# Kernel tuning notes

Measured on AMD Instinct MI355X. Metric: run time of the kernel, lower is better.

Reference implementation:

```python
import jax, jax.numpy as jnp
import numpy as np

N, D, H, DK, DEG = 8192, 512, 8, 64, 16
E = N * DEG
M = N


def setup_inputs() -> dict:
    key = jax.random.key(0)
    ks = jax.random.split(key, 12)
    x = jax.random.normal(ks[0], (N, D), dtype=jnp.float32)
    # every node has DEG neighbors -> sorted row index, random cols
    row_index = jnp.repeat(jnp.arange(N, dtype=jnp.int64), DEG)
    col_index = jax.random.randint(ks[1], (E,), 0, M, dtype=jnp.int64)
    to_col_index = jax.random.randint(ks[2], (M,), 0, N, dtype=jnp.int64)
    att_bias = 0.1 * jax.random.normal(ks[3], (H, E), dtype=jnp.float32)
    pos = 10.0 * jax.random.uniform(ks[4], (N, 3), dtype=jnp.float32)
    col_pos = 10.0 * jax.random.uniform(ks[5], (M, 3), dtype=jnp.float32)
    dist = jnp.linalg.norm(col_pos[col_index] - pos[row_index], axis=-1)
    s = 1.0 / np.sqrt(D)
    Wq = s * jax.random.normal(ks[6], (H, DK, D), dtype=jnp.float32)
    Wqv = s * jax.random.normal(ks[7], (H, 3, D), dtype=jnp.float32)
    Wk = s * jax.random.normal(ks[8], (H, DK, D), dtype=jnp.float32)
    Wv = s * jax.random.normal(ks[9], (H, DK, D), dtype=jnp.float32)
    Wout = s * jax.random.normal(ks[10], (D, D + 4 * H), dtype=jnp.float32)
    bout = jnp.zeros((D,), dtype=jnp.float32)
    return {"x": x, "row_index": row_index, "col_index": col_index,
            "to_col_index": to_col_index, "att_bias": att_bias, "dist": dist,
            "pos": pos, "col_pos": col_pos, "Wq": Wq, "Wqv": Wqv, "Wk": Wk,
            "Wv": Wv, "Wout": Wout, "bout": bout}


def reference(x, row_index, col_index, to_col_index, att_bias, dist, pos,
              col_pos, Wq, Wqv, Wk, Wv, Wout, bout):
    n = x.shape[0]
    dk = Wq.shape[1]
    scale = 1.0 / jnp.sqrt(jnp.asarray(dk, x.dtype))
    # per-head projections: [H, N, dk]
    q = jnp.einsum('nd,hkd->hnk', x, Wq) * scale
    qv = jnp.einsum('nd,hkd->hnk', x, Wqv)              # [H, N, 3]
    kx = jnp.einsum('nd,hkd->hnk', x, Wk)[:, to_col_index]  # [H, M, dk]
    vx = jnp.einsum('nd,hkd->hnk', x, Wv)[:, to_col_index]
    # gather per edge -> [E, H, *]
    qe = q[:, row_index].transpose(1, 0, 2)
    ke = kx[:, col_index].transpose(1, 0, 2)
    qve = qv[:, row_index].transpose(1, 0, 2)           # [E, H, 3]
    rel = col_pos[col_index] - pos[row_index]           # [E, 3]
    dist_e = jnp.where(dist == 0, jnp.inf, dist)        # masked_fill(dist==0, inf)
    # angular = qv_row . col_pos_col - qv_row . pos_row = qv_row . rel
    angular = jnp.einsum('ehc,ec->eh', qve, rel)
    logit = jnp.einsum('ehk,ehk->eh', qe, ke) + att_bias.T + angular / dist_e[:, None]
    # sparse (per-row segment) softmax
    m = jax.ops.segment_max(logit, row_index, num_segments=n)
    p = jnp.exp(logit - m[row_index])
    s = jax.ops.segment_sum(p, row_index, num_segments=n)
    att = p / s[row_index]                              # [E, H]
    natt = att / dist_e[:, None]
    dst_vec = jax.ops.segment_sum(natt[:, :, None] * col_pos[col_index][:, None, :],
                                  row_index, num_segments=n)   # [N, H, 3]
    avg_inv_dist = jax.ops.segment_sum(natt, row_index, num_segments=n)  # [N, H]
    src_vec = avg_inv_dist[:, :, None] * pos[:, None, :]
    diff = dst_vec - src_vec
    feat3 = diff / jnp.maximum(jnp.linalg.norm(diff, axis=-1, keepdims=True), 1e-12)
    ve = vx[:, col_index].transpose(1, 0, 2)            # [E, H, dk]
    y = jax.ops.segment_sum(att[:, :, None] * ve, row_index, num_segments=n)  # [N, H, dk]
    feat = jnp.concatenate([y, feat3, avg_inv_dist[:, :, None]], axis=-1)
    feat = feat.reshape(n, -1)                          # [N, H*(dk+4)]
    return feat @ Wout.T + bout
```

## Files before the change

kernel.cpp:

```cpp
#include <hip/hip_runtime.h>
#include <math.h>

#define N_NODES 8192
#define D_FEAT  512
#define DEG     16
#define E_EDGES (N_NODES * DEG)
#define FEAT_W  576
#define FEAT_USED 544
#define OUT_W   512
#define QKV_W   1664

typedef unsigned short u16;
typedef __attribute__((ext_vector_type(8))) short short8;
typedef __attribute__((ext_vector_type(8))) unsigned short us8;
typedef __attribute__((ext_vector_type(4))) float f32x4;

__device__ __forceinline__ u16 f2bf(float f) {
    union { float f; unsigned u; } c; c.f = f;
    unsigned u = c.u;
    unsigned r = u + 0x7FFFu + ((u >> 16) & 1u);
    return (u16)(r >> 16);
}
__device__ __forceinline__ float bf2f(u16 h) {
    union { unsigned u; float f; } c; c.u = ((unsigned)h) << 16;
    return c.f;
}

__device__ __forceinline__ void async16(const void* g, void* l) {
    __builtin_amdgcn_global_load_lds(
        (const __attribute__((address_space(1))) void*)g,
        (__attribute__((address_space(3))) void*)l, 16, 0, 0);
}

__global__ __launch_bounds__(256) void gemm_qkv(
    const u16* __restrict__ xh, const u16* __restrict__ Bfuse,
    u16* __restrict__ qkv)
{
    __shared__ u16 smem[128 * 64 * 2];
    u16* sA = smem;
    u16* sB = smem + 128 * 64;

    const int tid = threadIdx.x;
    const int flat = blockIdx.x;
    const int xcd = flat & 7;
    const int rr  = flat >> 3;
    const int bm  = (xcd + 8 * (rr / 13)) * 128;
    const int bn  = (rr % 13) * 128;

    const int wave = tid >> 6;
    const int lane = tid & 63;
    const int wr   = (wave >> 1) * 64;
    const int wc   = (wave & 1) * 64;
    const int lrow = lane & 15;
    const int quad = lane >> 4;

    f32x4 acc[4][4];
    #pragma unroll
    for (int i = 0; i < 4; ++i)
        #pragma unroll
        for (int j = 0; j < 4; ++j) {
            f32x4 z = {0.f, 0.f, 0.f, 0.f};
            acc[i][j] = z;
        }

    for (int k0 = 0; k0 < 512; k0 += 64) {
        #pragma unroll
        for (int i = 0; i < 4; ++i) {
            const int lin = i * 256 + tid;
            const int row = lin >> 3;
            const int seg = ((lin & 7) ^ (row & 7)) << 3;
            async16(xh    + (size_t)(bm + row) * 512 + k0 + seg, sA + (lin << 3));
            async16(Bfuse + (size_t)(bn + row) * 512 + k0 + seg, sB + (lin << 3));
        }
        __syncthreads();

        #pragma unroll
        for (int ko = 0; ko < 64; ko += 32) {
            const int cbase = ko >> 3;
            short8 a_h[4], b_h[4];
            #pragma unroll
            for (int t = 0; t < 4; ++t) {
                const int ra = wr + t * 16 + lrow;
                const int rb = wc + t * 16 + lrow;
                a_h[t] = *(const short8*)&sA[ra * 64 + (((cbase + quad) ^ (ra & 7)) << 3)];
                b_h[t] = *(const short8*)&sB[rb * 64 + (((cbase + quad) ^ (rb & 7)) << 3)];
            }
            #pragma unroll
            for (int mt = 0; mt < 4; ++mt)
                #pragma unroll
                for (int nt = 0; nt < 4; ++nt)
                    acc[mt][nt] = __builtin_amdgcn_mfma_f32_16x16x32_bf16(
                        a_h[mt], b_h[nt], acc[mt][nt], 0, 0, 0);
        }
        __syncthreads();
    }

    #pragma unroll
    for (int nt = 0; nt < 4; ++nt) {
        const int col = bn + wc + nt * 16 + lrow;
        #pragma unroll
        for (int mt = 0; mt < 4; ++mt)
            #pragma unroll
            for (int r = 0; r < 4; ++r) {
                const int row = bm + wr + mt * 16 + quad * 4 + r;
                qkv[(size_t)row * QKV_W + col] = f2bf(acc[mt][nt][r]);
            }
    }
}

__global__ __launch_bounds__(256) void gemm_out(
    const u16* __restrict__ feat, const u16* __restrict__ Woth,
    const float* __restrict__ bout, float* __restrict__ out)
{
    __shared__ u16 smem[64 * 64 + 128 * 64];
    u16* sA = smem;
    u16* sB = smem + 64 * 64;

    const int tid = threadIdx.x;
    const int flat = blockIdx.x;
    const int xcd = flat & 7;
    const int rr  = flat >> 3;
    const int bm  = (xcd + 8 * (rr / 4)) * 64;
    const int bn  = (rr % 4) * 128;

    const int wave = tid >> 6;
    const int lane = tid & 63;
    const int wr   = (wave >> 1) * 32;
    const int wc   = (wave & 1) * 64;
    const int lrow = lane & 15;
    const int quad = lane >> 4;

    f32x4 acc[2][4];
    #pragma unroll
    for (int i = 0; i < 2; ++i)
        #pragma unroll
        for (int j = 0; j < 4; ++j) {
            f32x4 z = {0.f, 0.f, 0.f, 0.f};
            acc[i][j] = z;
        }

    for (int k0 = 0; k0 < FEAT_W; k0 += 64) {
        #pragma unroll
        for (int i = 0; i < 2; ++i) {
            const int lin = i * 256 + tid;
            const int row = lin >> 3;
            const int seg = ((lin & 7) ^ (row & 7)) << 3;
            async16(feat + (size_t)(bm + row) * FEAT_W + k0 + seg, sA + (lin << 3));
        }
        #pragma unroll
        for (int i = 0; i < 4; ++i) {
            const int lin = i * 256 + tid;
            const int row = lin >> 3;
            const int seg = ((lin & 7) ^ (row & 7)) << 3;
            async16(Woth + (size_t)(bn + row) * FEAT_W + k0 + seg, sB + (lin << 3));
        }
        __syncthreads();

        #pragma unroll
        for (int ko = 0; ko < 64; ko += 32) {
            const int cbase = ko >> 3;
            short8 a_h[2], b_h[4];
            #pragma unroll
            for (int t = 0; t < 2; ++t) {
                const int ra = wr + t * 16 + lrow;
                a_h[t] = *(const short8*)&sA[ra * 64 + (((cbase + quad) ^ (ra & 7)) << 3)];
            }
            #pragma unroll
            for (int t = 0; t < 4; ++t) {
                const int rb = wc + t * 16 + lrow;
                b_h[t] = *(const short8*)&sB[rb * 64 + (((cbase + quad) ^ (rb & 7)) << 3)];
            }
            #pragma unroll
            for (int mt = 0; mt < 2; ++mt)
                #pragma unroll
                for (int nt = 0; nt < 4; ++nt)
                    acc[mt][nt] = __builtin_amdgcn_mfma_f32_16x16x32_bf16(
                        a_h[mt], b_h[nt], acc[mt][nt], 0, 0, 0);
        }
        __syncthreads();
    }

    #pragma unroll
    for (int nt = 0; nt < 4; ++nt) {
        const int col = bn + wc + nt * 16 + lrow;
        const float bb = bout[col];
        #pragma unroll
        for (int mt = 0; mt < 2; ++mt)
            #pragma unroll
            for (int r = 0; r < 4; ++r) {
                const int row = bm + wr + mt * 16 + quad * 4 + r;
                out[(size_t)row * OUT_W + col] = acc[mt][nt][r] + bb;
            }
    }
}

__global__ __launch_bounds__(256) void prep_kernel(
    const float* __restrict__ x,
    const float* __restrict__ Wq, const float* __restrict__ Wk,
    const float* __restrict__ Wv, const float* __restrict__ Wqv,
    const float* __restrict__ Wout,
    u16* __restrict__ xh, u16* __restrict__ B, u16* __restrict__ Woth)
{
    const int b = blockIdx.x;
    const int tid = threadIdx.x;
    if (b < 4096) {
        const int i = b * 256 + tid;
        const float4 v = ((const float4*)x)[i];
        ushort4 h;
        h.x = f2bf(v.x); h.y = f2bf(v.y); h.z = f2bf(v.z); h.w = f2bf(v.w);
        ((ushort4*)xh)[i] = h;
    } else if (b < 4928) {
        const int idx = (b - 4096) * 256 + tid;
        const int row = idx >> 7;
        const int c4  = idx & 127;
        float4 v = make_float4(0.f, 0.f, 0.f, 0.f);
        float scale = 1.f;
        if (row < 512) {
            v = *(const float4*)(Wq + (size_t)row * 512 + c4 * 4);
            scale = 0.125f;
        } else if (row < 1024) {
            v = *(const float4*)(Wk + (size_t)(row - 512) * 512 + c4 * 4);
        } else if (row < 1536) {
            v = *(const float4*)(Wv + (size_t)(row - 1024) * 512 + c4 * 4);
        } else if (row < 1560) {
            v = *(const float4*)(Wqv + (size_t)(row - 1536) * 512 + c4 * 4);
        }
        ushort4 h;
        h.x = f2bf(v.x * scale); h.y = f2bf(v.y * scale);
        h.z = f2bf(v.z * scale); h.w = f2bf(v.w * scale);
        ((ushort4*)B)[idx] = h;
    } else {
        const int i = (b - 4928) * 256 + tid;
        const int row = i / (FEAT_W / 4);
        const int c4  = i % (FEAT_W / 4);
        float4 v = make_float4(0.f, 0.f, 0.f, 0.f);
        if (c4 < FEAT_USED / 4)
            v = *(const float4*)(Wout + (size_t)row * FEAT_USED + c4 * 4);
        ushort4 h;
        h.x = f2bf(v.x); h.y = f2bf(v.y); h.z = f2bf(v.z); h.w = f2bf(v.w);
        ((ushort4*)Woth)[i] = h;
    }
}

__global__ __launch_bounds__(256) void edge_kernel(
    const u16* __restrict__ qkv,
    const int* __restrict__ col_index, const int* __restrict__ to_col,
    const float* __restrict__ att_bias, const float* __restrict__ dist,
    const float* __restrict__ pos, const float* __restrict__ col_pos,
    u16* __restrict__ feat)
{
    __shared__ float sLog[2][2][8][8];
    __shared__ float sY[2][512];
    __shared__ float sV[2][8][4];

    const int wave4 = threadIdx.x >> 6;
    const int nb = wave4 >> 1;
    const int w  = wave4 & 1;
    const int lane = threadIdx.x & 63;
    const int n = blockIdx.x * 2 + nb;
    const int h = lane >> 3;
    const int sub = lane & 7;
    const int hoff = lane * 8;

    const size_t qbase = (size_t)n * QKV_W;

    float qf[8];
    {
        const us8 qu = *(const us8*)(qkv + qbase + hoff);
        #pragma unroll
        for (int i = 0; i < 8; ++i) qf[i] = bf2f(qu[i]);
    }
    float qv0, qv1, qv2;
    {
        const float qvl = bf2f(qkv[qbase + 1536 + (lane < 24 ? lane : 0)]);
        qv0 = __shfl(qvl, h * 3 + 0);
        qv1 = __shfl(qvl, h * 3 + 1);
        qv2 = __shfl(qvl, h * 3 + 2);
    }
    const float px = pos[3 * n + 0], py = pos[3 * n + 1], pz = pos[3 * n + 2];

    const int j8 = lane & 7;
    const int e0 = n * DEG + w * 8 + j8;
    const int c_l  = col_index[e0];
    const int cc_l = to_col[c_l];
    const float d_l = dist[e0];
    const float invd_l = (d_l == 0.f) ? 0.f : (1.f / d_l);
    const float rx_l = col_pos[3 * c_l + 0] - px;
    const float ry_l = col_pos[3 * c_l + 1] - py;
    const float rz_l = col_pos[3 * c_l + 2] - pz;

    const float b_own = att_bias[(size_t)h * E_EDGES + n * DEG + w * 8 + sub];

    float logit[8];
    #pragma unroll
    for (int j = 0; j < 8; ++j) {
        const int cc = __shfl(cc_l, j);
        const us8 ku = *(const us8*)(qkv + (size_t)cc * QKV_W + 512 + hoff);
        float dot = 0.f;
        #pragma unroll
        for (int i = 0; i < 8; ++i) dot += qf[i] * bf2f(ku[i]);
        dot += __shfl_xor(dot, 1, 8);
        dot += __shfl_xor(dot, 2, 8);
        dot += __shfl_xor(dot, 4, 8);
        const float invd = __shfl(invd_l, j);
        const float ang = qv0 * __shfl(rx_l, j) + qv1 * __shfl(ry_l, j)
                        + qv2 * __shfl(rz_l, j);
        const float bj = __shfl(b_own, j, 8);
        logit[j] = dot + bj + ang * invd;
    }

    if (sub == 0) {
        #pragma unroll
        for (int j = 0; j < 8; ++j) sLog[nb][w][h][j] = logit[j];
    }
    __syncthreads();
    float lo[8];
    #pragma unroll
    for (int j = 0; j < 8; ++j) lo[j] = sLog[nb][1 - w][h][j];

    float m = logit[0];
    #pragma unroll
    for (int j = 1; j < 8; ++j) m = fmaxf(m, logit[j]);
    #pragma unroll
    for (int j = 0; j < 8; ++j) m = fmaxf(m, lo[j]);
    float s = 0.f;
    #pragma unroll
    for (int j = 0; j < 8; ++j) { logit[j] = __expf(logit[j] - m); s += logit[j]; }
    #pragma unroll
    for (int j = 0; j < 8; ++j) s += __expf(lo[j] - m);
    const float inv_s = 1.f / s;

    float y[8] = {0.f, 0.f, 0.f, 0.f, 0.f, 0.f, 0.f, 0.f};
    float dx = 0.f, dy = 0.f, dz = 0.f, aid = 0.f;
    #pragma unroll
    for (int j = 0; j < 8; ++j) {
        const float a = logit[j] * inv_s;
        const int cc = __shfl(cc_l, j);
        const us8 vu = *(const us8*)(qkv + (size_t)cc * QKV_W + 1024 + hoff);
        #pragma unroll
        for (int i = 0; i < 8; ++i) y[i] += a * bf2f(vu[i]);
        const float na = a * __shfl(invd_l, j);
        dx += na * __shfl(rx_l, j);
        dy += na * __shfl(ry_l, j);
        dz += na * __shfl(rz_l, j);
        aid += na;
    }

    if (w == 0) {
        #pragma unroll
        for (int i = 0; i < 8; ++i) sY[nb][hoff + i] = y[i];
        if (sub == 0) {
            sV[nb][h][0] = dx; sV[nb][h][1] = dy;
            sV[nb][h][2] = dz; sV[nb][h][3] = aid;
        }
    }
    __syncthreads();
    if (w == 1) {
        #pragma unroll
        for (int i = 0; i < 8; ++i) y[i] += sY[nb][hoff + i];

        u16* f = feat + (size_t)n * FEAT_W + h * 68;
        ushort4 o0, o1;
        o0.x = f2bf(y[0]); o0.y = f2bf(y[1]); o0.z = f2bf(y[2]); o0.w = f2bf(y[3]);
        o1.x = f2bf(y[4]); o1.y = f2bf(y[5]); o1.z = f2bf(y[6]); o1.w = f2bf(y[7]);
        *(ushort4*)(f + sub * 8 + 0) = o0;
        *(ushort4*)(f + sub * 8 + 4) = o1;
        if (sub == 0) {
            dx += sV[nb][h][0]; dy += sV[nb][h][1];
            dz += sV[nb][h][2]; aid += sV[nb][h][3];
            const float nrm = sqrtf(dx * dx + dy * dy + dz * dz);
            const float rn = 1.f / fmaxf(nrm, 1e-12f);
            ushort4 ex;
            ex.x = f2bf(dx * rn); ex.y = f2bf(dy * rn);
            ex.z = f2bf(dz * rn); ex.w = f2bf(aid);
            *(ushort4*)(f + 64) = ex;
        }
    }
}

extern "C" void kernel_launch(void* const* d_in, const int* in_sizes, int n_in,
                              void* d_out, int out_size, void* d_ws, size_t ws_size,
                              hipStream_t stream)
{
    const float* x         = (const float*)d_in[0];
    const int*   col_index = (const int*)d_in[2];
    const int*   to_col    = (const int*)d_in[3];
    const float* att_bias  = (const float*)d_in[4];
    const float* dist      = (const float*)d_in[5];
    const float* pos       = (const float*)d_in[6];
    const float* col_pos   = (const float*)d_in[7];
    const float* Wq        = (const float*)d_in[8];
    const float* Wqv       = (const float*)d_in[9];
    const float* Wk        = (const float*)d_in[10];
    const float* Wv        = (const float*)d_in[11];
    const float* Wout      = (const float*)d_in[12];
    const float* bout      = (const float*)d_in[13];
    float* out = (float*)d_out;

    char* ws = (char*)d_ws;
    u16* qkv   = (u16*)(ws + 0);
    u16* xh    = (u16*)(ws + 27262976);
    u16* Bfuse = (u16*)(ws + 35651584);
    u16* Woth  = (u16*)(ws + 37355520);
    u16* feat  = (u16*)(ws + 37945344);

    dim3 blk(256);

    hipLaunchKernelGGL(prep_kernel, dim3(5216), blk, 0, stream,
                       x, Wq, Wk, Wv, Wqv, Wout, xh, Bfuse, Woth);

    hipLaunchKernelGGL(gemm_qkv, dim3(832), blk, 0, stream, xh, Bfuse, qkv);

    hipLaunchKernelGGL(edge_kernel, dim3(N_NODES / 2), blk, 0, stream,
                       qkv, col_index, to_col, att_bias, dist, pos, col_pos, feat);

    hipLaunchKernelGGL(gemm_out, dim3(512), blk, 0, stream,
                       feat, Woth, bout, out);
}
```

Measured before the change: 163.9 us.

## Rewrite QKV GEMM with 256x256 tiles and 4-stage async LDS pipeline

The QKV projection GEMM moves from 128x128 tiles with 256 threads to 256x256 tiles with 512 threads. It adds a four-buffer global-to-LDS prefetch ring with explicit waitcnt and barrier scheduling, and raises wave priority around the MFMA bursts. The aim is to overlap global loads with matrix math, cut per-tile sync stalls, and increase operand reuse. The fused weight buffer is padded to 1792 rows so N divides by 256, which adds some wasted compute on the padding columns and increases register pressure.

```diff
diff --git a/kernel.cpp b/kernel.cpp
--- a/kernel.cpp
+++ b/kernel.cpp
@@ -9,6 +9,7 @@
 #define FEAT_USED 544
 #define OUT_W   512
 #define QKV_W   1664
+#define BF_ROWS 1792
 
 typedef unsigned short u16;
 typedef __attribute__((ext_vector_type(8))) short short8;
@@ -32,79 +33,128 @@
         (__attribute__((address_space(3))) void*)l, 16, 0, 0);
 }
 
-__global__ __launch_bounds__(256) void gemm_qkv(
+__global__ __launch_bounds__(512, 2) void gemm_qkv(
     const u16* __restrict__ xh, const u16* __restrict__ Bfuse,
     u16* __restrict__ qkv)
 {
-    __shared__ u16 smem[128 * 64 * 2];
-    u16* sA = smem;
-    u16* sB = smem + 128 * 64;
-
-    const int tid = threadIdx.x;
-    const int flat = blockIdx.x;
-    const int xcd = flat & 7;
-    const int rr  = flat >> 3;
-    const int bm  = (xcd + 8 * (rr / 13)) * 128;
-    const int bn  = (rr % 13) * 128;
-
-    const int wave = tid >> 6;
+    __shared__ u16 ldsA[4][256 * 32];
+    __shared__ u16 ldsB[4][256 * 32];
+
+    const int tid  = threadIdx.x;
+    const int wid  = tid >> 6;
     const int lane = tid & 63;
-    const int wr   = (wave >> 1) * 64;
-    const int wc   = (wave & 1) * 64;
+    const int wm   = wid >> 2;
+    const int wn   = wid & 3;
     const int lrow = lane & 15;
     const int quad = lane >> 4;
 
-    f32x4 acc[4][4];
-    #pragma unroll
-    for (int i = 0; i < 4; ++i)
+    const int flat = blockIdx.x;
+    const int wg   = (flat & 7) * 28 + (flat >> 3);
+    const int bm   = (wg / 7) * 256;
+    const int bn   = (wg % 7) * 256;
+
+    const u16* gA = xh    + (size_t)bm * 512;
+    const u16* gB = Bfuse + (size_t)bn * 512;
+
+    const int c0 = tid,       r0 = c0 >> 2;
+    const int c1 = 512 + tid, r1 = c1 >> 2;
+    const int o0 = (((c0 & 3) ^ ((r0 >> 1) & 3)) << 3);
+    const int o1 = (((c1 & 3) ^ ((r1 >> 1) & 3)) << 3);
+
+#define STAGE_A(s) do {                                                      \
+        u16* _d = &ldsA[(s) & 3][0];                                         \
+        async16(gA + (size_t)r0 * 512 + (s) * 32 + o0, _d + c0 * 8);         \
+        async16(gA + (size_t)r1 * 512 + (s) * 32 + o1, _d + c1 * 8);         \
+    } while (0)
+#define STAGE_B(s) do {                                                      \
+        u16* _d = &ldsB[(s) & 3][0];                                         \
+        async16(gB + (size_t)r0 * 512 + (s) * 32 + o0, _d + c0 * 8);         \
+        async16(gB + (size_t)r1 * 512 + (s) * 32 + o1, _d + c1 * 8);         \
+    } while (0)
+
+    f32x4 acc[8][4];
+    #pragma unroll
+    for (int i = 0; i < 8; ++i)
         #pragma unroll
         for (int j = 0; j < 4; ++j) {
             f32x4 z = {0.f, 0.f, 0.f, 0.f};
             acc[i][j] = z;
         }
 
-    for (int k0 = 0; k0 < 512; k0 += 64) {
-        #pragma unroll
-        for (int i = 0; i < 4; ++i) {
-            const int lin = i * 256 + tid;
-            const int row = lin >> 3;
-            const int seg = ((lin & 7) ^ (row & 7)) << 3;
-            async16(xh    + (size_t)(bm + row) * 512 + k0 + seg, sA + (lin << 3));
-            async16(Bfuse + (size_t)(bn + row) * 512 + k0 + seg, sB + (lin << 3));
-        }
-        __syncthreads();
-
-        #pragma unroll
-        for (int ko = 0; ko < 64; ko += 32) {
-            const int cbase = ko >> 3;
-            short8 a_h[4], b_h[4];
-            #pragma unroll
-            for (int t = 0; t < 4; ++t) {
-                const int ra = wr + t * 16 + lrow;
-                const int rb = wc + t * 16 + lrow;
-                a_h[t] = *(const short8*)&sA[ra * 64 + (((cbase + quad) ^ (ra & 7)) << 3)];
-                b_h[t] = *(const short8*)&sB[rb * 64 + (((cbase + quad) ^ (rb & 7)) << 3)];
-            }
-            #pragma unroll
-            for (int mt = 0; mt < 4; ++mt)
+    STAGE_A(0); STAGE_B(0);
+    STAGE_A(1); STAGE_B(1);
+    STAGE_A(2); STAGE_B(2);
+    asm volatile("s_waitcnt vmcnt(8)" ::: "memory");
+    __builtin_amdgcn_s_barrier();
+
+    #pragma unroll
+    for (int s = 0; s < 16; ++s) {
+        const int b = s & 3;
+        const u16* sa = &ldsA[b][0];
+        const u16* sb = &ldsB[b][0];
+        short8 av[4], bv[4], av2[4];
+
+        #pragma unroll
+        for (int m = 0; m < 4; ++m) {
+            const int row = wm * 128 + m * 16 + lrow;
+            av[m] = *(const short8*)&sa[row * 32 + ((quad ^ ((row >> 1) & 3)) << 3)];
+        }
+        #pragma unroll
+        for (int n = 0; n < 4; ++n) {
+            const int row = wn * 64 + n * 16 + lrow;
+            bv[n] = *(const short8*)&sb[row * 32 + ((quad ^ ((row >> 1) & 3)) << 3)];
+        }
+        if (s < 13) STAGE_A(s + 3);
+        __builtin_amdgcn_s_barrier();
+        asm volatile("s_waitcnt lgkmcnt(0)" ::: "memory");
+        __builtin_amdgcn_sched_barrier(0);
+        __builtin_amdgcn_s_setprio(1);
+        #pragma unroll
+        for (int m = 0; m < 4; ++m)
+            #pragma unroll
+            for (int n = 0; n < 4; ++n)
+                acc[m][n] = __builtin_amdgcn_mfma_f32_16x16x32_bf16(
+                    av[m], bv[n], acc[m][n], 0, 0, 0);
+        __builtin_amdgcn_s_setprio(0);
+        __builtin_amdgcn_s_barrier();
+
+        #pragma unroll
+        for (int m = 0; m < 4; ++m) {
+            const int row = wm * 128 + 64 + m * 16 + lrow;
+            av2[m] = *(const short8*)&sa[row * 32 + ((quad ^ ((row >> 1) & 3)) << 3)];
+        }
+        if (s < 13) STAGE_B(s + 3);
+        __builtin_amdgcn_s_barrier();
+        asm volatile("s_waitcnt lgkmcnt(0)" ::: "memory");
+        __builtin_amdgcn_sched_barrier(0);
+        __builtin_amdgcn_s_setprio(1);
+        #pragma unroll
+        for (int m = 0; m < 4; ++m)
+            #pragma unroll
+            for (int n = 0; n < 4; ++n)
+                acc[4 + m][n] = __builtin_amdgcn_mfma_f32_16x16x32_bf16(
+                    av2[m], bv[n], acc[4 + m][n], 0, 0, 0);
+        __builtin_amdgcn_s_setprio(0);
+        if (s < 13)       asm volatile("s_waitcnt vmcnt(8)" ::: "memory");
+        else if (s == 13) asm volatile("s_waitcnt vmcnt(4)" ::: "memory");
+        else if (s == 14) asm volatile("s_waitcnt vmcnt(0)" ::: "memory");
+        __builtin_amdgcn_s_barrier();
+    }
+#undef STAGE_A
+#undef STAGE_B
+
+    #pragma unroll
+    for (int np = 0; np < 4; ++np) {
+        const int col = bn + wn * 64 + np * 16 + lrow;
+        if (col < 1560) {
+            #pragma unroll
+            for (int mp = 0; mp < 8; ++mp)
                 #pragma unroll
-                for (int nt = 0; nt < 4; ++nt)
-                    acc[mt][nt] = __builtin_amdgcn_mfma_f32_16x16x32_bf16(
-                        a_h[mt], b_h[nt], acc[mt][nt], 0, 0, 0);
-        }
-        __syncthreads();
-    }
-
-    #pragma unroll
-    for (int nt = 0; nt < 4; ++nt) {
-        const int col = bn + wc + nt * 16 + lrow;
-        #pragma unroll
-        for (int mt = 0; mt < 4; ++mt)
-            #pragma unroll
-            for (int r = 0; r < 4; ++r) {
-                const int row = bm + wr + mt * 16 + quad * 4 + r;
-                qkv[(size_t)row * QKV_W + col] = f2bf(acc[mt][nt][r]);
-            }
+                for (int r = 0; r < 4; ++r) {
+                    const int row = bm + wm * 128 + mp * 16 + quad * 4 + r;
+                    qkv[(size_t)row * QKV_W + col] = f2bf(acc[mp][np][r]);
+                }
+        }
     }
 }
 
@@ -209,7 +259,7 @@
         ushort4 h;
         h.x = f2bf(v.x); h.y = f2bf(v.y); h.z = f2bf(v.z); h.w = f2bf(v.w);
         ((ushort4*)xh)[i] = h;
-    } else if (b < 4928) {
+    } else if (b < 4992) {
         const int idx = (b - 4096) * 256 + tid;
         const int row = idx >> 7;
         const int c4  = idx & 127;
@@ -230,7 +280,7 @@
         h.z = f2bf(v.z * scale); h.w = f2bf(v.w * scale);
         ((ushort4*)B)[idx] = h;
     } else {
-        const int i = (b - 4928) * 256 + tid;
+        const int i = (b - 4992) * 256 + tid;
         const int row = i / (FEAT_W / 4);
         const int c4  = i % (FEAT_W / 4);
         float4 v = make_float4(0.f, 0.f, 0.f, 0.f);
@@ -401,15 +451,16 @@
     u16* qkv   = (u16*)(ws + 0);
     u16* xh    = (u16*)(ws + 27262976);
     u16* Bfuse = (u16*)(ws + 35651584);
-    u16* Woth  = (u16*)(ws + 37355520);
-    u16* feat  = (u16*)(ws + 37945344);
+    u16* Woth  = (u16*)(ws + 37486592);
+    u16* feat  = (u16*)(ws + 38076416);
 
     dim3 blk(256);
 
-    hipLaunchKernelGGL(prep_kernel, dim3(5216), blk, 0, stream,
+    hipLaunchKernelGGL(prep_kernel, dim3(5280), blk, 0, stream,
                        x, Wq, Wk, Wv, Wqv, Wout, xh, Bfuse, Woth);
 
-    hipLaunchKernelGGL(gemm_qkv, dim3(832), blk, 0, stream, xh, Bfuse, qkv);
+    hipLaunchKernelGGL(gemm_qkv, dim3(224), dim3(512), 0, stream,
+                       xh, Bfuse, qkv);
 
     hipLaunchKernelGGL(edge_kernel, dim3(N_NODES / 2), blk, 0, stream,
                        qkv, col_index, to_col, att_bias, dist, pos, col_pos, feat);
```

Result: no change. 165.2 us (+0.8%).

## Rewrite QKV GEMM as register-resident B with direct global A loads

Applied to the files above, without the earlier changes.

Replaces the LDS-tiled 128x128 QKV GEMM with a scheme where each wave holds a 16-column slice of the fused weight matrix across all of K in registers. It then streams 16-row A fragments straight from global memory, with no LDS and no barriers. The weight buffer is padded to 1792 rows so the 25x64 column tiling fits, writes are masked past column 1560, and the prep kernel and workspace offsets are updated to match. The aim is to remove LDS traffic and synchronisation, at the cost of heavier register use and uncoalesced, repeated global reads of A across column blocks.

```diff
diff --git a/kernel.cpp b/kernel.cpp
--- a/kernel.cpp
+++ b/kernel.cpp
@@ -9,6 +9,7 @@
 #define FEAT_USED 544
 #define OUT_W   512
 #define QKV_W   1664
+#define BF_ROWS 1792
 
 typedef unsigned short u16;
 typedef __attribute__((ext_vector_type(8))) short short8;
@@ -36,75 +37,53 @@
     const u16* __restrict__ xh, const u16* __restrict__ Bfuse,
     u16* __restrict__ qkv)
 {
-    __shared__ u16 smem[128 * 64 * 2];
-    u16* sA = smem;
-    u16* sB = smem + 128 * 64;
-
-    const int tid = threadIdx.x;
-    const int flat = blockIdx.x;
-    const int xcd = flat & 7;
-    const int rr  = flat >> 3;
-    const int bm  = (xcd + 8 * (rr / 13)) * 128;
-    const int bn  = (rr % 13) * 128;
-
+    const int tid  = threadIdx.x;
     const int wave = tid >> 6;
     const int lane = tid & 63;
-    const int wr   = (wave >> 1) * 64;
-    const int wc   = (wave & 1) * 64;
     const int lrow = lane & 15;
     const int quad = lane >> 4;
 
-    f32x4 acc[4][4];
-    #pragma unroll
-    for (int i = 0; i < 4; ++i)
-        #pragma unroll
-        for (int j = 0; j < 4; ++j) {
-            f32x4 z = {0.f, 0.f, 0.f, 0.f};
-            acc[i][j] = z;
-        }
-
-    for (int k0 = 0; k0 < 512; k0 += 64) {
-        #pragma unroll
-        for (int i = 0; i < 4; ++i) {
-            const int lin = i * 256 + tid;
-            const int row = lin >> 3;
-            const int seg = ((lin & 7) ^ (row & 7)) << 3;
-            async16(xh    + (size_t)(bm + row) * 512 + k0 + seg, sA + (lin << 3));
-            async16(Bfuse + (size_t)(bn + row) * 512 + k0 + seg, sB + (lin << 3));
-        }
-        __syncthreads();
-
-        #pragma unroll
-        for (int ko = 0; ko < 64; ko += 32) {
-            const int cbase = ko >> 3;
-            short8 a_h[4], b_h[4];
-            #pragma unroll
-            for (int t = 0; t < 4; ++t) {
-                const int ra = wr + t * 16 + lrow;
-                const int rb = wc + t * 16 + lrow;
-                a_h[t] = *(const short8*)&sA[ra * 64 + (((cbase + quad) ^ (ra & 7)) << 3)];
-                b_h[t] = *(const short8*)&sB[rb * 64 + (((cbase + quad) ^ (rb & 7)) << 3)];
-            }
-            #pragma unroll
-            for (int mt = 0; mt < 4; ++mt)
-                #pragma unroll
-                for (int nt = 0; nt < 4; ++nt)
-                    acc[mt][nt] = __builtin_amdgcn_mfma_f32_16x16x32_bf16(
-                        a_h[mt], b_h[nt], acc[mt][nt], 0, 0, 0);
-        }
-        __syncthreads();
-    }
-
-    #pragma unroll
-    for (int nt = 0; nt < 4; ++nt) {
-        const int col = bn + wc + nt * 16 + lrow;
-        #pragma unroll
-        for (int mt = 0; mt < 4; ++mt)
-            #pragma unroll
-            for (int r = 0; r < 4; ++r) {
-                const int row = bm + wr + mt * 16 + quad * 4 + r;
-                qkv[(size_t)row * QKV_W + col] = f2bf(acc[mt][nt][r]);
-            }
+    const int flat = blockIdx.x;
+    const int xcd  = flat & 7;
+    const int rr   = flat >> 3;
+    const int bm   = (xcd * 4 + rr / 25) * 256;
+    const int bn   = (rr % 25) * 64;
+
+    const int coln = bn + wave * 16 + lrow;
+    short8 b[16];
+    {
+        const u16* gB = Bfuse + (size_t)coln * 512 + quad * 8;
+        #pragma unroll
+        for (int ks = 0; ks < 16; ++ks)
+            b[ks] = *(const short8*)(gB + ks * 32);
+    }
+
+    const u16* gA = xh + (size_t)(bm + lrow) * 512 + quad * 8;
+    u16* gC = qkv + (size_t)(bm + quad * 4) * QKV_W + coln;
+    const bool wr_ok = (coln < 1560);
+
+    #pragma unroll 2
+    for (int mt = 0; mt < 16; ++mt) {
+        const u16* ga = gA + (size_t)(mt * 16) * 512;
+        short8 a[16];
+        #pragma unroll
+        for (int ks = 0; ks < 16; ++ks)
+            a[ks] = *(const short8*)(ga + ks * 32);
+
+        f32x4 ae = {0.f, 0.f, 0.f, 0.f};
+        f32x4 ao = {0.f, 0.f, 0.f, 0.f};
+        #pragma unroll
+        for (int ks = 0; ks < 16; ks += 2) {
+            ae = __builtin_amdgcn_mfma_f32_16x16x32_bf16(a[ks],     b[ks],     ae, 0, 0, 0);
+            ao = __builtin_amdgcn_mfma_f32_16x16x32_bf16(a[ks + 1], b[ks + 1], ao, 0, 0, 0);
+        }
+
+        if (wr_ok) {
+            u16* gc = gC + (size_t)(mt * 16) * QKV_W;
+            #pragma unroll
+            for (int r = 0; r < 4; ++r)
+                gc[(size_t)r * QKV_W] = f2bf(ae[r] + ao[r]);
+        }
     }
 }
 
@@ -209,7 +188,7 @@
         ushort4 h;
         h.x = f2bf(v.x); h.y = f2bf(v.y); h.z = f2bf(v.z); h.w = f2bf(v.w);
         ((ushort4*)xh)[i] = h;
-    } else if (b < 4928) {
+    } else if (b < 4992) {
         const int idx = (b - 4096) * 256 + tid;
         const int row = idx >> 7;
         const int c4  = idx & 127;
@@ -230,7 +209,7 @@
         h.z = f2bf(v.z * scale); h.w = f2bf(v.w * scale);
         ((ushort4*)B)[idx] = h;
     } else {
-        const int i = (b - 4928) * 256 + tid;
+        const int i = (b - 4992) * 256 + tid;
         const int row = i / (FEAT_W / 4);
         const int c4  = i % (FEAT_W / 4);
         float4 v = make_float4(0.f, 0.f, 0.f, 0.f);
@@ -401,15 +380,15 @@
     u16* qkv   = (u16*)(ws + 0);
     u16* xh    = (u16*)(ws + 27262976);
     u16* Bfuse = (u16*)(ws + 35651584);
-    u16* Woth  = (u16*)(ws + 37355520);
-    u16* feat  = (u16*)(ws + 37945344);
+    u16* Woth  = (u16*)(ws + 37486592);
+    u16* feat  = (u16*)(ws + 38076416);
 
     dim3 blk(256);
 
-    hipLaunchKernelGGL(prep_kernel, dim3(5216), blk, 0, stream,
+    hipLaunchKernelGGL(prep_kernel, dim3(5280), blk, 0, stream,
                        x, Wq, Wk, Wv, Wqv, Wout, xh, Bfuse, Woth);
 
-    hipLaunchKernelGGL(gemm_qkv, dim3(832), blk, 0, stream, xh, Bfuse, qkv);
+    hipLaunchKernelGGL(gemm_qkv, dim3(800), blk, 0, stream, xh, Bfuse, qkv);
 
     hipLaunchKernelGGL(edge_kernel, dim3(N_NODES / 2), blk, 0, stream,
                        qkv, col_index, to_col, att_bias, dist, pos, col_pos, feat);
```

After: 262.4 us. 60.1% more time.
